# Optimization experiments

Hardware: AMD Instinct MI355X
Metric: run time of the kernel (lower is better)

The kernel has to match this reference:

```python
import jax, jax.numpy as jnp
import numpy as np

BN_EPS = 1e-05


def setup_inputs() -> dict:
    key = jax.random.key(0)
    ks = jax.random.split(key, 6)
    B, IN, OUT = 8192, 4096, 4096
    x = jax.random.normal(ks[0], (B, IN), dtype=jnp.float32)
    weight = jax.random.normal(ks[1], (OUT, IN), dtype=jnp.float32)
    bn_gamma = jax.random.uniform(ks[2], (OUT,), dtype=jnp.float32, minval=0.5, maxval=1.5)
    bn_beta = jax.random.normal(ks[3], (OUT,), dtype=jnp.float32)
    bn_mean = jax.random.normal(ks[4], (OUT,), dtype=jnp.float32)
    bn_var = jax.random.uniform(ks[5], (OUT,), dtype=jnp.float32, minval=0.1, maxval=2.0)
    return {"x": x, "weight": weight, "bn_gamma": bn_gamma, "bn_beta": bn_beta,
            "bn_mean": bn_mean, "bn_var": bn_var}


def reference(x, weight, bn_gamma, bn_beta, bn_mean, bn_var):
    # deterministic +/-1 binarization of activations and weights (eval path)
    x_bin = jnp.sign(x)
    w_bin = jnp.sign(weight)
    # binary linear: [B, IN] @ [IN, OUT] -> [B, OUT]
    out = jnp.einsum('bi,oi->bo', x_bin, w_bin)
    # exact (non-folded) BatchNorm using running stats
    std = jnp.sqrt(bn_var + BN_EPS)
    out = (out - bn_mean) / std * bn_gamma + bn_beta
    return out
```

## Files before the change

### kernel.cpp

```cpp
#include <hip/hip_runtime.h>
#include <stdint.h>
#include <stddef.h>


#define BN_EPS 1e-5f
typedef int   v4i  __attribute__((ext_vector_type(4)));
typedef float v16f __attribute__((ext_vector_type(16)));
typedef unsigned int u32;

__global__ void bn_prep_kernel(const float* __restrict__ g, const float* __restrict__ b,
                               const float* __restrict__ m, const float* __restrict__ v,
                               float* __restrict__ scale, float* __restrict__ bias, int n) {
  int i = blockIdx.x * blockDim.x + threadIdx.x;
  if (i >= n) return;
  float s = g[i] * rsqrtf(v[i] + BN_EPS);
  scale[i] = s;
  bias[i] = b[i] - m[i] * s;
}

__global__ __launch_bounds__(256) void pack_sign_fp4_kernel(
    const uint4* __restrict__ in, uint4* __restrict__ outp, int n32) {
  int t = blockIdx.x * blockDim.x + threadIdx.x;
  if (t >= n32) return;
  const uint4* p = in + (size_t)t * 8;
  u32 w[4];
#pragma unroll
  for (int j = 0; j < 4; ++j) {
    uint4 u0 = p[2 * j];
    uint4 u1 = p[2 * j + 1];
    u32 h0 = 0x2222u | ((u0.x >> 28) & 0x8u) | (((u0.y >> 28) & 0x8u) << 4)
                     | (((u0.z >> 28) & 0x8u) << 8) | (((u0.w >> 28) & 0x8u) << 12);
    u32 h1 = 0x2222u | ((u1.x >> 28) & 0x8u) | (((u1.y >> 28) & 0x8u) << 4)
                     | (((u1.z >> 28) & 0x8u) << 8) | (((u1.w >> 28) & 0x8u) << 12);
    w[j] = h0 | (h1 << 16);
  }
  uint4 o; o.x = w[0]; o.y = w[1]; o.z = w[2]; o.w = w[3];
  outp[t] = o;
}


#define BAR() asm volatile("s_barrier" ::: "memory")
#define WAITV8() asm volatile("s_waitcnt vmcnt(8)" ::: "memory")
#define WAITV4() asm volatile("s_waitcnt vmcnt(4)" ::: "memory")
#define WAITV0() asm volatile("s_waitcnt vmcnt(0)" ::: "memory")
#define LGKM0() asm volatile("s_waitcnt lgkmcnt(0)" ::: "memory")

#define MFMA4(accv, av, bv) \
  asm("v_mfma_f32_32x32x64_f8f6f4 %0, %1, %2, %0 cbsz:4 blgp:4" \
      : "+v"(accv) : "v"(av), "v"(bv))

__global__ __launch_bounds__(512, 2) void bgemm_fp4(
    const int8_t* __restrict__ A4, const int8_t* __restrict__ B4,
    const float* __restrict__ scale, const float* __restrict__ bias,
    float* __restrict__ out, int M, int N, int RB ) {
  __shared__ __align__(16) int8_t lds[131072];

  const int tid = threadIdx.x;
  const int lane = tid & 63;
  const int wid = tid >> 6;
  const int wm = wid >> 2;
  const int wn = wid & 3;

  const int nbx = N >> 8;
  const int nwg = (M >> 8) * nbx;
  const int cpx = nwg >> 3;
  const int bid = (int)blockIdx.x;
  const int swz = (bid & 7) * cpx + (bid >> 3);
  const int row0 = (swz / nbx) << 8;
  const int col0 = (swz % nbx) << 8;

  const int rl = lane & 31;
  const int hi = lane >> 5;
  const int key = (lane >> 1) & 3;
  const int g0 = ((hi) ^ key) << 4;
  const int g1 = ((2 | hi) ^ key) << 4;
  const int aoff = (wm * 128 + rl) * 64;
  const int boff = (wn * 64 + rl) * 64;

  const int srow = wid * 16 + (lane >> 2);
  const int sch = (((lane & 3) ^ ((lane >> 3) & 3)) << 4);
  const int ldw = wid << 10;

  const size_t rstr = (size_t)128 * RB;
  const int8_t* aSt = A4 + (size_t)(row0 + srow) * RB + sch;
  const int8_t* bSt = B4 + (size_t)(col0 + srow) * RB + sch;

  v16f acc[4][2];
#pragma unroll
  for (int i = 0; i < 4; ++i)
#pragma unroll
    for (int n = 0; n < 2; ++n)
#pragma unroll
      for (int e = 0; e < 16; ++e) acc[i][n][e] = 0.0f;

#define STAGE(s) do {                                                                 \
  const int bb_ = ((s) & 3) * 16384;                                                  \
  __builtin_amdgcn_global_load_lds(                                                   \
      (const __attribute__((address_space(1))) uint32_t*)(aSt + (size_t)(s) * 64),    \
      (__attribute__((address_space(3))) uint32_t*)(lds + bb_ + ldw), 16, 0, 0);      \
  __builtin_amdgcn_global_load_lds(                                                   \
      (const __attribute__((address_space(1))) uint32_t*)(aSt + rstr + (size_t)(s) * 64), \
      (__attribute__((address_space(3))) uint32_t*)(lds + bb_ + 8192 + ldw), 16, 0, 0); \
  __builtin_amdgcn_global_load_lds(                                                   \
      (const __attribute__((address_space(1))) uint32_t*)(bSt + (size_t)(s) * 64),    \
      (__attribute__((address_space(3))) uint32_t*)(lds + 65536 + bb_ + ldw), 16, 0, 0); \
  __builtin_amdgcn_global_load_lds(                                                   \
      (const __attribute__((address_space(1))) uint32_t*)(bSt + rstr + (size_t)(s) * 64), \
      (__attribute__((address_space(3))) uint32_t*)(lds + 65536 + bb_ + 8192 + ldw), 16, 0, 0); \
} while (0)

#define COMPUTE(q) do {                                                               \
  const int8_t* bp_ = lds + 65536 + (q) * 16384 + boff;                               \
  v4i B00 = *(const v4i*)(bp_ + g0);       v4i B01 = *(const v4i*)(bp_ + 2048 + g0);  \
  v4i B10 = *(const v4i*)(bp_ + g1);       v4i B11 = *(const v4i*)(bp_ + 2048 + g1);  \
  __builtin_amdgcn_s_setprio(1);                                                      \
  _Pragma("unroll")                                                                   \
  for (int mt_ = 0; mt_ < 4; ++mt_) {                                                 \
    const int8_t* ap_ = lds + (q) * 16384 + aoff + mt_ * 2048;                        \
    v4i A0 = *(const v4i*)(ap_ + g0);                                                 \
    v4i A1 = *(const v4i*)(ap_ + g1);                                                 \
    MFMA4(acc[mt_][0], A0, B00);                                                      \
    MFMA4(acc[mt_][1], A0, B01);                                                      \
    MFMA4(acc[mt_][0], A1, B10);                                                      \
    MFMA4(acc[mt_][1], A1, B11);                                                      \
  }                                                                                   \
  __builtin_amdgcn_s_setprio(0);                                                      \
} while (0)

  const int NT = RB >> 6;

  STAGE(0); STAGE(1); STAGE(2);
  WAITV8();
  BAR();

  for (int t = 0; t < NT - 3; ++t) {
    STAGE(t + 3);
    COMPUTE(t & 3);
    LGKM0();
    WAITV8();
    BAR();
  }
  COMPUTE((NT - 3) & 3); LGKM0(); WAITV4(); BAR();
  COMPUTE((NT - 2) & 3); LGKM0(); WAITV0(); BAR();
  COMPUTE((NT - 1) & 3);
  asm volatile("s_nop 7\n\ts_nop 7" :::);

  const int cb = col0 + wn * 64 + rl;
  float scv[2], biv[2];
#pragma unroll
  for (int n = 0; n < 2; ++n) {
    scv[n] = scale[cb + n * 32];
    biv[n] = bias[cb + n * 32];
  }
#pragma unroll
  for (int mt = 0; mt < 4; ++mt) {
    const int rb = row0 + wm * 128 + mt * 32 + 4 * hi;
#pragma unroll
    for (int nt = 0; nt < 2; ++nt) {
      const int c = cb + nt * 32;
#pragma unroll
      for (int reg = 0; reg < 16; ++reg) {
        const int r = rb + (reg & 3) + 8 * (reg >> 2);
        out[(size_t)r * N + c] = fmaf(acc[mt][nt][reg], scv[nt], biv[nt]);
      }
    }
  }

#undef STAGE
#undef COMPUTE
}

extern "C" void kernel_launch(void* const* d_in, const int* in_sizes, int n_in,
                              void* d_out, int out_size, void* d_ws, size_t ws_size,
                              hipStream_t stream) {
  const float* x = (const float*)d_in[0];
  const float* w = (const float*)d_in[1];
  const float* gamma = (const float*)d_in[2];
  const float* beta = (const float*)d_in[3];
  const float* mean = (const float*)d_in[4];
  const float* var = (const float*)d_in[5];
  float* out = (float*)d_out;

  const int OUT = in_sizes[2];
  const int IN = in_sizes[1] / OUT;
  const int B = in_sizes[0] / IN;
  const int RB = IN / 2;

  int8_t* a4 = (int8_t*)d_ws;
  int8_t* b4 = a4 + (size_t)B * RB;
  float* scale = (float*)(b4 + (size_t)OUT * RB);
  float* bias = scale + OUT;

  const int n32x = B * (IN / 32);
  const int n32w = OUT * (IN / 32);
  pack_sign_fp4_kernel<<<(n32x + 255) / 256, 256, 0, stream>>>(
      (const uint4*)x, (uint4*)a4, n32x);
  pack_sign_fp4_kernel<<<(n32w + 255) / 256, 256, 0, stream>>>(
      (const uint4*)w, (uint4*)b4, n32w);
  bn_prep_kernel<<<(OUT + 255) / 256, 256, 0, stream>>>(
      gamma, beta, mean, var, scale, bias, OUT);

  dim3 grid((B >> 8) * (OUT >> 8));
  bgemm_fp4<<<grid, 512, 0, stream>>>(a4, b4, scale, bias, out, B, OUT, RB);
}
```

Baseline: 130.3 us.

## Switch FP4 GEMM to 16x16x128 MFMA and double-step the pipeline

Replaces the 32x32x64 FP4 MFMA with the 16x16x128 variant. Each wave now computes an 8x4 grid of 16x16 tiles, with one A fragment and four B fragments loaded from LDS per K-step, and the epilogue is remapped to match. The main loop now issues two stages and runs two computes per barrier, waiting for all loads (vmcnt 0) instead of keeping three stages in flight. This cuts the barrier count but reduces prefetch depth, so global-load latency may be exposed more.

```diff
diff --git a/kernel.cpp b/kernel.cpp
--- a/kernel.cpp
+++ b/kernel.cpp
@@ -4,8 +4,8 @@
 
 
 #define BN_EPS 1e-5f
-typedef int   v4i  __attribute__((ext_vector_type(4)));
-typedef float v16f __attribute__((ext_vector_type(16)));
+typedef int   v4i __attribute__((ext_vector_type(4)));
+typedef float v4f __attribute__((ext_vector_type(4)));
 typedef unsigned int u32;
 
 __global__ void bn_prep_kernel(const float* __restrict__ g, const float* __restrict__ b,
@@ -40,16 +40,14 @@
 
 
 #define BAR() asm volatile("s_barrier" ::: "memory")
-#define WAITV8() asm volatile("s_waitcnt vmcnt(8)" ::: "memory")
-#define WAITV4() asm volatile("s_waitcnt vmcnt(4)" ::: "memory")
 #define WAITV0() asm volatile("s_waitcnt vmcnt(0)" ::: "memory")
 #define LGKM0() asm volatile("s_waitcnt lgkmcnt(0)" ::: "memory")
 
-#define MFMA4(accv, av, bv) \
-  asm("v_mfma_f32_32x32x64_f8f6f4 %0, %1, %2, %0 cbsz:4 blgp:4" \
+#define MFMA16x16(accv, av, bv) \
+  asm("v_mfma_f32_16x16x128_f8f6f4 %0, %1, %2, %0 cbsz:4 blgp:4" \
       : "+v"(accv) : "v"(av), "v"(bv))
 
-__global__ __launch_bounds__(512, 2) void bgemm_fp4(
+__global__ __launch_bounds__(512, 2) void bgemm_fp4_16(
     const int8_t* __restrict__ A4, const int8_t* __restrict__ B4,
     const float* __restrict__ scale, const float* __restrict__ bias,
     float* __restrict__ out, int M, int N, int RB ) {
@@ -69,13 +67,10 @@
   const int row0 = (swz / nbx) << 8;
   const int col0 = (swz % nbx) << 8;
 
-  const int rl = lane & 31;
-  const int hi = lane >> 5;
-  const int key = (lane >> 1) & 3;
-  const int g0 = ((hi) ^ key) << 4;
-  const int g1 = ((2 | hi) ^ key) << 4;
-  const int aoff = (wm * 128 + rl) * 64;
-  const int boff = (wn * 64 + rl) * 64;
+  const int ln15 = lane & 15;
+  const int kcs = (((lane >> 4) ^ ((ln15 >> 1) & 3)) << 4);
+  const int aoff = (wm * 128 + ln15) * 64 + kcs;
+  const int boff = (wn * 64 + ln15) * 64 + kcs;
 
   const int srow = wid * 16 + (lane >> 2);
   const int sch = (((lane & 3) ^ ((lane >> 3) & 3)) << 4);
@@ -85,13 +80,11 @@
   const int8_t* aSt = A4 + (size_t)(row0 + srow) * RB + sch;
   const int8_t* bSt = B4 + (size_t)(col0 + srow) * RB + sch;
 
-  v16f acc[4][2];
+  v4f acc[8][4];
 #pragma unroll
-  for (int i = 0; i < 4; ++i)
+  for (int i = 0; i < 8; ++i)
 #pragma unroll
-    for (int n = 0; n < 2; ++n)
-#pragma unroll
-      for (int e = 0; e < 16; ++e) acc[i][n][e] = 0.0f;
+    for (int n = 0; n < 4; ++n) { v4f z = {0.f, 0.f, 0.f, 0.f}; acc[i][n] = z; }
 
 #define STAGE(s) do {                                                                 \
   const int bb_ = ((s) & 3) * 16384;                                                  \
@@ -110,59 +103,58 @@
 } while (0)
 
 #define COMPUTE(q) do {                                                               \
+  const int8_t* ap_ = lds + (q) * 16384 + aoff;                                       \
   const int8_t* bp_ = lds + 65536 + (q) * 16384 + boff;                               \
-  v4i B00 = *(const v4i*)(bp_ + g0);       v4i B01 = *(const v4i*)(bp_ + 2048 + g0);  \
-  v4i B10 = *(const v4i*)(bp_ + g1);       v4i B11 = *(const v4i*)(bp_ + 2048 + g1);  \
+  v4i Bv0 = *(const v4i*)(bp_);        v4i Bv1 = *(const v4i*)(bp_ + 1024);           \
+  v4i Bv2 = *(const v4i*)(bp_ + 2048); v4i Bv3 = *(const v4i*)(bp_ + 3072);           \
   __builtin_amdgcn_s_setprio(1);                                                      \
   _Pragma("unroll")                                                                   \
-  for (int mt_ = 0; mt_ < 4; ++mt_) {                                                 \
-    const int8_t* ap_ = lds + (q) * 16384 + aoff + mt_ * 2048;                        \
-    v4i A0 = *(const v4i*)(ap_ + g0);                                                 \
-    v4i A1 = *(const v4i*)(ap_ + g1);                                                 \
-    MFMA4(acc[mt_][0], A0, B00);                                                      \
-    MFMA4(acc[mt_][1], A0, B01);                                                      \
-    MFMA4(acc[mt_][0], A1, B10);                                                      \
-    MFMA4(acc[mt_][1], A1, B11);                                                      \
+  for (int m_ = 0; m_ < 8; ++m_) {                                                    \
+    v4i Av = *(const v4i*)(ap_ + m_ * 1024);                                          \
+    MFMA16x16(acc[m_][0], Av, Bv0);                                                   \
+    MFMA16x16(acc[m_][1], Av, Bv1);                                                   \
+    MFMA16x16(acc[m_][2], Av, Bv2);                                                   \
+    MFMA16x16(acc[m_][3], Av, Bv3);                                                   \
   }                                                                                   \
   __builtin_amdgcn_s_setprio(0);                                                      \
 } while (0)
 
   const int NT = RB >> 6;
 
-  STAGE(0); STAGE(1); STAGE(2);
-  WAITV8();
+  STAGE(0); STAGE(1);
+  WAITV0();
   BAR();
 
-  for (int t = 0; t < NT - 3; ++t) {
-    STAGE(t + 3);
+  int t = 0;
+  for (; t < NT - 2; t += 2) {
+    STAGE(t + 2); STAGE(t + 3);
     COMPUTE(t & 3);
+    COMPUTE((t + 1) & 3);
     LGKM0();
-    WAITV8();
+    WAITV0();
     BAR();
   }
-  COMPUTE((NT - 3) & 3); LGKM0(); WAITV4(); BAR();
-  COMPUTE((NT - 2) & 3); LGKM0(); WAITV0(); BAR();
+  COMPUTE((NT - 2) & 3);
   COMPUTE((NT - 1) & 3);
   asm volatile("s_nop 7\n\ts_nop 7" :::);
 
-  const int cb = col0 + wn * 64 + rl;
-  float scv[2], biv[2];
+  const int cw = col0 + wn * 64;
+  float scv[4], biv[4];
 #pragma unroll
-  for (int n = 0; n < 2; ++n) {
-    scv[n] = scale[cb + n * 32];
-    biv[n] = bias[cb + n * 32];
+  for (int n = 0; n < 4; ++n) {
+    int c = cw + n * 16 + ln15;
+    scv[n] = scale[c];
+    biv[n] = bias[c];
   }
 #pragma unroll
-  for (int mt = 0; mt < 4; ++mt) {
-    const int rb = row0 + wm * 128 + mt * 32 + 4 * hi;
+  for (int i = 0; i < 8; ++i) {
+    const int r0 = row0 + wm * 128 + i * 16 + ((lane >> 4) << 2);
 #pragma unroll
-    for (int nt = 0; nt < 2; ++nt) {
-      const int c = cb + nt * 32;
+    for (int reg = 0; reg < 4; ++reg) {
+      float* orow = out + (size_t)(r0 + reg) * N;
 #pragma unroll
-      for (int reg = 0; reg < 16; ++reg) {
-        const int r = rb + (reg & 3) + 8 * (reg >> 2);
-        out[(size_t)r * N + c] = fmaf(acc[mt][nt][reg], scv[nt], biv[nt]);
-      }
+      for (int n = 0; n < 4; ++n)
+        orow[cw + n * 16 + ln15] = fmaf(acc[i][n][reg], scv[n], biv[n]);
     }
   }
 
@@ -201,5 +193,5 @@
       gamma, beta, mean, var, scale, bias, OUT);
 
   dim3 grid((B >> 8) * (OUT >> 8));
-  bgemm_fp4<<<grid, 512, 0, stream>>>(a4, b4, scale, bias, out, B, OUT, RB);
+  bgemm_fp4_16<<<grid, 512, 0, stream>>>(a4, b4, scale, bias, out, B, OUT, RB);
 }
```

New measurement: 133.9 us. +2.8%, slower.
